# Kernel tuning notes

Hardware: AMD Instinct MI355X
Metric: run time of the kernel (lower is better)

Reference implementation:

```python
import jax, jax.numpy as jnp
import numpy as np

B, U, V = 2, 32, 2048
IN_DIM, STATE, CODE = 256, 512, 256
H, HD = 8, 64
INNER = H * HD  # 512
HID = STATE     # ffn capacity_factor = 1.0


def layernorm(x, g, b, eps=1e-5):
    mu = jnp.mean(x, axis=-1, keepdims=True)
    var = jnp.var(x, axis=-1, keepdims=True)
    return (x - mu) * jax.lax.rsqrt(var + eps) * g + b


def setup_inputs() -> dict:
    key = jax.random.key(0)
    ks = jax.random.split(key, 24)
    s = 0.02
    inp = {
        'receiver_states': jax.random.normal(ks[0], (B, U, STATE), jnp.float32),
        'receiver_signatures': jax.random.normal(ks[1], (B, U, 64), jnp.float32),
        'receiver_codes': jax.random.normal(ks[2], (B, U, CODE), jnp.float32),
        'sender_states': jax.random.normal(ks[3], (B, V, IN_DIM), jnp.float32),
        # layernorms
        'ln_s_g': jnp.ones((IN_DIM,), jnp.float32), 'ln_s_b': jnp.zeros((IN_DIM,), jnp.float32),
        'ln_r_g': jnp.ones((STATE,), jnp.float32), 'ln_r_b': jnp.zeros((STATE,), jnp.float32),
        # ModFC query: in=STATE out=INNER ctx=CODE
        'Wq': jax.random.normal(ks[4], (INNER, STATE), jnp.float32) * s,
        'bq': jnp.zeros((INNER,), jnp.float32),
        'Cq': jax.random.normal(ks[5], (STATE, CODE), jnp.float32) * s,
        # ModFC key/value: in=IN_DIM out=INNER ctx=CODE
        'Wk': jax.random.normal(ks[6], (INNER, IN_DIM), jnp.float32) * s,
        'bk': jnp.zeros((INNER,), jnp.float32),
        'Ck': jax.random.normal(ks[7], (IN_DIM, CODE), jnp.float32) * s,
        'Wv': jax.random.normal(ks[8], (INNER, IN_DIM), jnp.float32) * s,
        'bv': jnp.zeros((INNER,), jnp.float32),
        'Cv': jax.random.normal(ks[9], (IN_DIM, CODE), jnp.float32) * s,
        # exit ModFC: in=INNER out=STATE ctx=CODE
        'We': jax.random.normal(ks[10], (STATE, INNER), jnp.float32) * s,
        'be': jnp.zeros((STATE,), jnp.float32),
        'Ce': jax.random.normal(ks[11], (INNER, CODE), jnp.float32) * s,
        'ls_attn': jnp.ones((STATE,), jnp.float32) * 1.0,
        # FFN
        'ln_f_g': jnp.ones((STATE,), jnp.float32), 'ln_f_b': jnp.zeros((STATE,), jnp.float32),
        'W1': jax.random.normal(ks[12], (HID, STATE), jnp.float32) * s,
        'b1': jnp.zeros((HID,), jnp.float32),
        'C1': jax.random.normal(ks[13], (STATE, CODE), jnp.float32) * s,
        'W2': jax.random.normal(ks[14], (STATE, HID), jnp.float32) * s,
        'b2': jnp.zeros((STATE,), jnp.float32),
        'C2': jax.random.normal(ks[15], (HID, CODE), jnp.float32) * s,
        'ls_ffn': jnp.ones((STATE,), jnp.float32) * 1e-6,
    }
    return inp


def reference(receiver_states, receiver_signatures, receiver_codes, sender_states,
              ln_s_g, ln_s_b, ln_r_g, ln_r_b,
              Wq, bq, Cq, Wk, bk, Ck, Wv, bv, Cv, We, be, Ce, ls_attn,
              ln_f_g, ln_f_b, W1, b1, C1, W2, b2, C2, ls_ffn):
    codes = receiver_codes  # (b,u,code)
    # --- ReadInAttention ---
    r_ln = layernorm(receiver_states, ln_r_g, ln_r_b)           # (b,u,state)
    s_ln = layernorm(sender_states, ln_s_g, ln_s_b)             # (b,v,in)
    # ModFC: y = linear(x * (1 + code @ C))
    # queries: (b,u,inner)
    q = jnp.einsum('bus,is->bui', r_ln * (1.0 + jnp.einsum('buc,sc->bus', codes, Cq)), Wq) + bq
    # per-receiver modulated senders: scale (b,u,in) broadcast over v
    scale_k = 1.0 + jnp.einsum('buc,ic->bui', codes, Ck)        # (b,u,in)
    scale_v = 1.0 + jnp.einsum('buc,ic->bui', codes, Cv)        # (b,u,in)
    mod_k = s_ln[:, :, None, :] * scale_k[:, None, :, :]        # (b,v,u,in)
    mod_v = s_ln[:, :, None, :] * scale_v[:, None, :, :]        # (b,v,u,in)
    keys = jnp.einsum('bvui,oi->bvuo', mod_k, Wk) + bk          # (b,v,u,inner)
    values = jnp.einsum('bvui,oi->bvuo', mod_v, Wv) + bv        # (b,v,u,inner)
    keys = keys.reshape(B, V, U, H, HD).transpose(0, 3, 2, 1, 4)    # (b,h,u,v,c)
    values = values.reshape(B, V, U, H, HD).transpose(0, 3, 2, 1, 4)
    qh = q.reshape(B, U, H, HD).transpose(0, 2, 1, 3)           # (b,h,u,c)
    scores = jnp.einsum('bhuc,bhuvc->bhuv', qh, keys) / np.sqrt(HD)
    attn = jax.nn.softmax(scores, axis=-1)
    msg = jnp.einsum('bhuv,bhuvc->bhuc', attn, values)          # (b,h,u,c)
    msg = msg.transpose(0, 2, 1, 3).reshape(B, U, INNER)        # (b,u,inner)
    msg = jnp.einsum('bui,oi->buo', msg * (1.0 + jnp.einsum('buc,ic->bui', codes, Ce)), We) + be
    attn_out = msg * ls_attn  # include_residual=False in read-in attention
    # --- ModFFN (residual) ---
    x = attn_out
    r = layernorm(x, ln_f_g, ln_f_b)
    h1 = jnp.einsum('bus,os->buo', r * (1.0 + jnp.einsum('buc,sc->bus', codes, C1)), W1) + b1
    h1 = jax.nn.gelu(h1, approximate=False)
    h2 = jnp.einsum('buh,oh->buo', h1 * (1.0 + jnp.einsum('buc,hc->buh', codes, C2)), W2) + b2
    out = x + h2 * ls_ffn
    return out
```

## Files before the change

### kernel.cpp

```cpp
#include <hip/hip_runtime.h>
#include <math.h>

#define B_ 2
#define U_ 32
#define V_ 2048
#define IN_ 256
#define ST_ 512
#define H_ 8
#define BU_ 64
#define NR_ 512

#define WS_SLN   0u
#define WS_SLNT  1048576u
#define WS_SCALE 2097152u
#define WS_T     2260992u
#define WS_CB    2392064u
#define WS_SSUMP 2392576u
#define WS_CTXP  2396672u
#define WS_AO    3445248u
#define WS_H2    3478016u
#define WS_AOP   3510784u

__device__ __forceinline__ float wsum(float v){
  #pragma unroll
  for(int m=32;m>0;m>>=1) v += __shfl_xor(v, m, 64);
  return v;
}

#define FMA4(A, t, S) { A.x += (t)*(S).x; A.y += (t)*(S).y; A.z += (t)*(S).z; A.w += (t)*(S).w; }

__global__ __launch_bounds__(256) void k_pre(const float* __restrict__ snd,
    const float* __restrict__ g, const float* __restrict__ bb,
    const float* __restrict__ codes,
    const float* __restrict__ Cq, const float* __restrict__ Ck, const float* __restrict__ Cv,
    const float* __restrict__ Ce, const float* __restrict__ C1, const float* __restrict__ C2,
    float* __restrict__ ws){
  __shared__ float tile[32][261];
  __shared__ float cds[8][256];
  const int tid = threadIdx.x;
  if(blockIdx.x < 128){
    const int wave = tid>>6, lane = tid&63;
    const int rowbase = blockIdx.x * 32;
    const int b = rowbase >> 11, vloc = rowbase & 2047;
    float4 gg  = *(const float4*)(g  + lane*4);
    float4 bbv = *(const float4*)(bb + lane*4);
    for(int it=0; it<8; ++it){
      int rl = it*4 + wave;
      int r  = rowbase + rl;
      float4 x = *(const float4*)(snd + (size_t)r*IN_ + lane*4);
      float s = x.x+x.y+x.z+x.w;
      float q = x.x*x.x+x.y*x.y+x.z*x.z+x.w*x.w;
      s = wsum(s); q = wsum(q);
      float mu = s*(1.0f/256.0f);
      float rv = rsqrtf(q*(1.0f/256.0f) - mu*mu + 1e-5f);
      float4 y;
      y.x = (x.x-mu)*rv*gg.x + bbv.x;
      y.y = (x.y-mu)*rv*gg.y + bbv.y;
      y.z = (x.z-mu)*rv*gg.z + bbv.z;
      y.w = (x.w-mu)*rv*gg.w + bbv.w;
      *(float4*)(ws + WS_SLN + (size_t)r*IN_ + lane*4) = y;
      tile[rl][lane*4+0] = y.x;
      tile[rl][lane*4+1] = y.y;
      tile[rl][lane*4+2] = y.z;
      tile[rl][lane*4+3] = y.w;
    }
    __syncthreads();
    const int vh = tid & 31;
    const int ibase = (tid >> 5);
    for(int it=0; it<32; ++it){
      int i = it*8 + ibase;
      ws[WS_SLNT + ((size_t)b*IN_ + i)*V_ + vloc + vh] = tile[vh][i];
    }
  } else {
    const int idx = blockIdx.x - 128;
    const int cg = idx % 40, bg = idx / 40;
    #pragma unroll
    for(int j=0;j<8;++j){
      int fi = j*256 + tid;
      cds[fi>>8][fi&255] = codes[(size_t)(bg*8)*256 + fi];
    }
    __syncthreads();
    const int q = tid & 3;
    const int col = cg*64 + (tid >> 2);
    const float* Cp; int loc;
    if(col < 512){ Cp = Cq; loc = col; }
    else if(col < 768){ Cp = Ck; loc = col - 512; }
    else if(col < 1024){ Cp = Cv; loc = col - 768; }
    else if(col < 1536){ Cp = Ce; loc = col - 1024; }
    else if(col < 2048){ Cp = C1; loc = col - 1536; }
    else { Cp = C2; loc = col - 2048; }
    const float4* wrow = (const float4*)(Cp + (size_t)loc*256 + q*64);
    float acc[8] = {0,0,0,0,0,0,0,0};
    #pragma unroll 4
    for(int i=0;i<16;++i){
      float4 w = wrow[i];
      #pragma unroll
      for(int k=0;k<8;++k){
        const float4 c = *(const float4*)(&cds[k][q*64 + i*4]);
        acc[k] += w.x*c.x + w.y*c.y + w.z*c.z + w.w*c.w;
      }
    }
    #pragma unroll
    for(int k=0;k<8;++k){
      acc[k] += __shfl_xor(acc[k], 1, 64);
      acc[k] += __shfl_xor(acc[k], 2, 64);
    }
    ws[WS_SCALE + (size_t)(bg*8 + q)*2560 + col]     = 1.0f + acc[q];
    ws[WS_SCALE + (size_t)(bg*8 + q + 4)*2560 + col] = 1.0f + acc[q+4];
  }
}

__global__ __launch_bounds__(256) void k_qt(const float* __restrict__ rst,
    const float* __restrict__ lg, const float* __restrict__ lb,
    const float* __restrict__ Wq, const float* __restrict__ bq,
    const float* __restrict__ Wk, const float* __restrict__ bk,
    float* __restrict__ ws){
  const int bu = blockIdx.x >> 3, h = blockIdx.x & 7;
  const int b = bu >> 5, u = bu & 31;
  const int r = (b*8 + h)*32 + u;
  const int tid = threadIdx.x, wave = tid>>6, lane = tid&63;
  __shared__ float xm[512];
  __shared__ float qv[64];
  __shared__ float red[4][65];
  __shared__ float rsm[4], rqm[4];
  float2 x2 = *(const float2*)(rst + (size_t)bu*512 + tid*2);
  float s = x2.x + x2.y, q = x2.x*x2.x + x2.y*x2.y;
  s = wsum(s); q = wsum(q);
  if(lane==0){ rsm[wave] = s; rqm[wave] = q; }
  __syncthreads();
  float S = rsm[0]+rsm[1]+rsm[2]+rsm[3];
  float Q = rqm[0]+rqm[1]+rqm[2]+rqm[3];
  float mu = S*(1.0f/512.0f);
  float rv = rsqrtf(Q*(1.0f/512.0f) - mu*mu + 1e-5f);
  const float* scal = ws + WS_SCALE + (size_t)bu*2560;
  xm[tid*2]   = ((x2.x-mu)*rv*lg[tid*2]   + lb[tid*2])   * scal[tid*2];
  xm[tid*2+1] = ((x2.y-mu)*rv*lg[tid*2+1] + lb[tid*2+1]) * scal[tid*2+1];
  __syncthreads();
  {
    const int o = tid & 63, sp = tid >> 6;
    const float4* wq = (const float4*)(Wq + (size_t)(h*64 + o)*512 + sp*128);
    const float* xp = xm + sp*128;
    float acc = 0.f;
    #pragma unroll 8
    for(int c4=0;c4<32;++c4){
      float4 w = wq[c4];
      acc += w.x*xp[c4*4] + w.y*xp[c4*4+1] + w.z*xp[c4*4+2] + w.w*xp[c4*4+3];
    }
    red[sp][o] = acc;
  }
  __syncthreads();
  if(tid < 64)
    qv[tid] = red[0][tid]+red[1][tid]+red[2][tid]+red[3][tid] + bq[h*64+tid];
  __syncthreads();
  if(tid < 64){
    float p = qv[tid] * bk[h*64+tid];
    p = wsum(p);
    if(tid==0) ws[WS_CB + r] = p;
  }
  {
    float acc = 0.f;
    #pragma unroll 4
    for(int d=0; d<64; ++d)
      acc += qv[d] * Wk[(size_t)(h*64+d)*256 + tid];
    ws[WS_T + (size_t)r*256 + tid] = acc * scal[512 + tid];
  }
}

__global__ __launch_bounds__(512) void k_scctx(const float* __restrict__ Tm, float* __restrict__ ws){
  const int rg = blockIdx.x >> 3, vc = blockIdx.x & 7;
  const int r0 = rg * 16;
  const int b  = rg >> 4;
  const int v0 = vc * 256;
  const int tid = threadIdx.x, lane = tid & 63;
  const int w  = __builtin_amdgcn_readfirstlane(tid >> 6);
  const int wr = w & 1, wk = w >> 1;
  const int rw8 = wr * 8;
  const int i0 = lane * 4;
  const int srow = tid >> 6;
  const int sf   = (tid & 63) * 4;

  __shared__ float P[16][256];
  __shared__ float stg[32][256];

  float4 a0={0,0,0,0},a1={0,0,0,0},a2={0,0,0,0},a3={0,0,0,0};
  float4 a4={0,0,0,0},a5={0,0,0,0},a6={0,0,0,0},a7={0,0,0,0};

  const float* Trow = Tm + (size_t)(r0 + rw8)*256;

  const float* p1base = ws + WS_SLNT + (size_t)b*IN_*V_ + v0;
  float4 g0,g1,g2,g3;
  g0 = *(const float4*)(p1base + (size_t)(srow    )*V_ + sf);
  g1 = *(const float4*)(p1base + (size_t)(srow+ 8)*V_ + sf);
  g2 = *(const float4*)(p1base + (size_t)(srow+16)*V_ + sf);
  g3 = *(const float4*)(p1base + (size_t)(srow+24)*V_ + sf);
  for(int s=0; s<8; ++s){
    __syncthreads();
    *(float4*)&stg[srow   ][sf] = g0;
    *(float4*)&stg[srow+ 8][sf] = g1;
    *(float4*)&stg[srow+16][sf] = g2;
    *(float4*)&stg[srow+24][sf] = g3;
    if(s < 7){
      const float* nb = p1base + (size_t)(s+1)*32*V_;
      g0 = *(const float4*)(nb + (size_t)(srow    )*V_ + sf);
      g1 = *(const float4*)(nb + (size_t)(srow+ 8)*V_ + sf);
      g2 = *(const float4*)(nb + (size_t)(srow+16)*V_ + sf);
      g3 = *(const float4*)(nb + (size_t)(srow+24)*V_ + sf);
    }
    const int kgA = s*32 + wk*8;
    float4 tA[8], tB[8];
    #pragma unroll
    for(int j=0;j<8;++j) tA[j] = *(const float4*)(Trow + (size_t)j*256 + kgA);
    __syncthreads();
    #pragma unroll
    for(int j=0;j<8;++j) tB[j] = *(const float4*)(Trow + (size_t)j*256 + kgA + 4);
    {
      const int kl = wk*8;
      float4 s0 = *(const float4*)&stg[kl+0][i0];
      float4 s1 = *(const float4*)&stg[kl+1][i0];
      float4 s2 = *(const float4*)&stg[kl+2][i0];
      float4 s3 = *(const float4*)&stg[kl+3][i0];
      FMA4(a0,tA[0].x,s0) FMA4(a0,tA[0].y,s1) FMA4(a0,tA[0].z,s2) FMA4(a0,tA[0].w,s3)
      FMA4(a1,tA[1].x,s0) FMA4(a1,tA[1].y,s1) FMA4(a1,tA[1].z,s2) FMA4(a1,tA[1].w,s3)
      FMA4(a2,tA[2].x,s0) FMA4(a2,tA[2].y,s1) FMA4(a2,tA[2].z,s2) FMA4(a2,tA[2].w,s3)
      FMA4(a3,tA[3].x,s0) FMA4(a3,tA[3].y,s1) FMA4(a3,tA[3].z,s2) FMA4(a3,tA[3].w,s3)
      FMA4(a4,tA[4].x,s0) FMA4(a4,tA[4].y,s1) FMA4(a4,tA[4].z,s2) FMA4(a4,tA[4].w,s3)
      FMA4(a5,tA[5].x,s0) FMA4(a5,tA[5].y,s1) FMA4(a5,tA[5].z,s2) FMA4(a5,tA[5].w,s3)
      FMA4(a6,tA[6].x,s0) FMA4(a6,tA[6].y,s1) FMA4(a6,tA[6].z,s2) FMA4(a6,tA[6].w,s3)
      FMA4(a7,tA[7].x,s0) FMA4(a7,tA[7].y,s1) FMA4(a7,tA[7].z,s2) FMA4(a7,tA[7].w,s3)
    }
    {
      const int kl = wk*8 + 4;
      float4 s0 = *(const float4*)&stg[kl+0][i0];
      float4 s1 = *(const float4*)&stg[kl+1][i0];
      float4 s2 = *(const float4*)&stg[kl+2][i0];
      float4 s3 = *(const float4*)&stg[kl+3][i0];
      FMA4(a0,tB[0].x,s0) FMA4(a0,tB[0].y,s1) FMA4(a0,tB[0].z,s2) FMA4(a0,tB[0].w,s3)
      FMA4(a1,tB[1].x,s0) FMA4(a1,tB[1].y,s1) FMA4(a1,tB[1].z,s2) FMA4(a1,tB[1].w,s3)
      FMA4(a2,tB[2].x,s0) FMA4(a2,tB[2].y,s1) FMA4(a2,tB[2].z,s2) FMA4(a2,tB[2].w,s3)
      FMA4(a3,tB[3].x,s0) FMA4(a3,tB[3].y,s1) FMA4(a3,tB[3].z,s2) FMA4(a3,tB[3].w,s3)
      FMA4(a4,tB[4].x,s0) FMA4(a4,tB[4].y,s1) FMA4(a4,tB[4].z,s2) FMA4(a4,tB[4].w,s3)
      FMA4(a5,tB[5].x,s0) FMA4(a5,tB[5].y,s1) FMA4(a5,tB[5].z,s2) FMA4(a5,tB[5].w,s3)
      FMA4(a6,tB[6].x,s0) FMA4(a6,tB[6].y,s1) FMA4(a6,tB[6].z,s2) FMA4(a6,tB[6].w,s3)
      FMA4(a7,tB[7].x,s0) FMA4(a7,tB[7].y,s1) FMA4(a7,tB[7].z,s2) FMA4(a7,tB[7].w,s3)
    }
  }
  __syncthreads();
  if(wk == 0){
    *(float4*)&P[rw8+0][i0]=a0; *(float4*)&P[rw8+1][i0]=a1;
    *(float4*)&P[rw8+2][i0]=a2; *(float4*)&P[rw8+3][i0]=a3;
    *(float4*)&P[rw8+4][i0]=a4; *(float4*)&P[rw8+5][i0]=a5;
    *(float4*)&P[rw8+6][i0]=a6; *(float4*)&P[rw8+7][i0]=a7;
  } else if(wk == 1){
    *(float4*)&stg[rw8+0][i0]=a0; *(float4*)&stg[rw8+1][i0]=a1;
    *(float4*)&stg[rw8+2][i0]=a2; *(float4*)&stg[rw8+3][i0]=a3;
    *(float4*)&stg[rw8+4][i0]=a4; *(float4*)&stg[rw8+5][i0]=a5;
    *(float4*)&stg[rw8+6][i0]=a6; *(float4*)&stg[rw8+7][i0]=a7;
  } else if(wk == 2){
    *(float4*)&stg[16+rw8+0][i0]=a0; *(float4*)&stg[16+rw8+1][i0]=a1;
    *(float4*)&stg[16+rw8+2][i0]=a2; *(float4*)&stg[16+rw8+3][i0]=a3;
    *(float4*)&stg[16+rw8+4][i0]=a4; *(float4*)&stg[16+rw8+5][i0]=a5;
    *(float4*)&stg[16+rw8+6][i0]=a6; *(float4*)&stg[16+rw8+7][i0]=a7;
  }
  __syncthreads();
  if(wk == 3){
    float4 av[8] = {a0,a1,a2,a3,a4,a5,a6,a7};
    #pragma unroll
    for(int j=0;j<8;++j){
      const int r = r0 + rw8 + j;
      const float cb = ws[WS_CB + r];
      float4 q0 = *(const float4*)&P[rw8+j][i0];
      float4 q1 = *(const float4*)&stg[rw8+j][i0];
      float4 q2 = *(const float4*)&stg[16+rw8+j][i0];
      float4 e;
      e.x = __expf((av[j].x+q0.x+q1.x+q2.x+cb)*0.125f);
      e.y = __expf((av[j].y+q0.y+q1.y+q2.y+cb)*0.125f);
      e.z = __expf((av[j].z+q0.z+q1.z+q2.z+cb)*0.125f);
      e.w = __expf((av[j].w+q0.w+q1.w+q2.w+cb)*0.125f);
      *(float4*)&P[rw8+j][i0] = e;
      float ss = wsum(e.x+e.y+e.z+e.w);
      if(lane==0) ws[WS_SSUMP + (size_t)r*8 + vc] = ss;
    }
  }

  a0=make_float4(0,0,0,0); a1=a0; a2=a0; a3=a0; a4=a0; a5=a0; a6=a0; a7=a0;
  const float* p2base = ws + WS_SLN + ((size_t)b*V_ + v0)*IN_;
  g0 = *(const float4*)(p2base + (size_t)(srow    )*IN_ + sf);
  g1 = *(const float4*)(p2base + (size_t)(srow+ 8)*IN_ + sf);
  g2 = *(const float4*)(p2base + (size_t)(srow+16)*IN_ + sf);
  g3 = *(const float4*)(p2base + (size_t)(srow+24)*IN_ + sf);
  for(int sv=0; sv<8; ++sv){
    __syncthreads();
    *(float4*)&stg[srow   ][sf] = g0;
    *(float4*)&stg[srow+ 8][sf] = g1;
    *(float4*)&stg[srow+16][sf] = g2;
    *(float4*)&stg[srow+24][sf] = g3;
    if(sv < 7){
      const float* nb = p2base + (size_t)(sv+1)*32*IN_;
      g0 = *(const float4*)(nb + (size_t)(srow    )*IN_ + sf);
      g1 = *(const float4*)(nb + (size_t)(srow+ 8)*IN_ + sf);
      g2 = *(const float4*)(nb + (size_t)(srow+16)*IN_ + sf);
      g3 = *(const float4*)(nb + (size_t)(srow+24)*IN_ + sf);
    }
    __syncthreads();
    {
      const int vl = wk*8, vg = sv*32 + vl;
      float4 p0_ = *(const float4*)&P[rw8+0][vg];
      float4 p1_ = *(const float4*)&P[rw8+1][vg];
      float4 p2_ = *(const float4*)&P[rw8+2][vg];
      float4 p3_ = *(const float4*)&P[rw8+3][vg];
      float4 p4_ = *(const float4*)&P[rw8+4][vg];
      float4 p5_ = *(const float4*)&P[rw8+5][vg];
      float4 p6_ = *(const float4*)&P[rw8+6][vg];
      float4 p7_ = *(const float4*)&P[rw8+7][vg];
      float4 s0 = *(const float4*)&stg[vl+0][i0];
      float4 s1 = *(const float4*)&stg[vl+1][i0];
      float4 s2 = *(const float4*)&stg[vl+2][i0];
      float4 s3 = *(const float4*)&stg[vl+3][i0];
      FMA4(a0,p0_.x,s0) FMA4(a0,p0_.y,s1) FMA4(a0,p0_.z,s2) FMA4(a0,p0_.w,s3)
      FMA4(a1,p1_.x,s0) FMA4(a1,p1_.y,s1) FMA4(a1,p1_.z,s2) FMA4(a1,p1_.w,s3)
      FMA4(a2,p2_.x,s0) FMA4(a2,p2_.y,s1) FMA4(a2,p2_.z,s2) FMA4(a2,p2_.w,s3)
      FMA4(a3,p3_.x,s0) FMA4(a3,p3_.y,s1) FMA4(a3,p3_.z,s2) FMA4(a3,p3_.w,s3)
      FMA4(a4,p4_.x,s0) FMA4(a4,p4_.y,s1) FMA4(a4,p4_.z,s2) FMA4(a4,p4_.w,s3)
      FMA4(a5,p5_.x,s0) FMA4(a5,p5_.y,s1) FMA4(a5,p5_.z,s2) FMA4(a5,p5_.w,s3)
      FMA4(a6,p6_.x,s0) FMA4(a6,p6_.y,s1) FMA4(a6,p6_.z,s2) FMA4(a6,p6_.w,s3)
      FMA4(a7,p7_.x,s0) FMA4(a7,p7_.y,s1) FMA4(a7,p7_.z,s2) FMA4(a7,p7_.w,s3)
    }
    {
      const int vl = wk*8 + 4, vg = sv*32 + vl;
      float4 p0_ = *(const float4*)&P[rw8+0][vg];
      float4 p1_ = *(const float4*)&P[rw8+1][vg];
      float4 p2_ = *(const float4*)&P[rw8+2][vg];
      float4 p3_ = *(const float4*)&P[rw8+3][vg];
      float4 p4_ = *(const float4*)&P[rw8+4][vg];
      float4 p5_ = *(const float4*)&P[rw8+5][vg];
      float4 p6_ = *(const float4*)&P[rw8+6][vg];
      float4 p7_ = *(const float4*)&P[rw8+7][vg];
      float4 s0 = *(const float4*)&stg[vl+0][i0];
      float4 s1 = *(const float4*)&stg[vl+1][i0];
      float4 s2 = *(const float4*)&stg[vl+2][i0];
      float4 s3 = *(const float4*)&stg[vl+3][i0];
      FMA4(a0,p0_.x,s0) FMA4(a0,p0_.y,s1) FMA4(a0,p0_.z,s2) FMA4(a0,p0_.w,s3)
      FMA4(a1,p1_.x,s0) FMA4(a1,p1_.y,s1) FMA4(a1,p1_.z,s2) FMA4(a1,p1_.w,s3)
      FMA4(a2,p2_.x,s0) FMA4(a2,p2_.y,s1) FMA4(a2,p2_.z,s2) FMA4(a2,p2_.w,s3)
      FMA4(a3,p3_.x,s0) FMA4(a3,p3_.y,s1) FMA4(a3,p3_.z,s2) FMA4(a3,p3_.w,s3)
      FMA4(a4,p4_.x,s0) FMA4(a4,p4_.y,s1) FMA4(a4,p4_.z,s2) FMA4(a4,p4_.w,s3)
      FMA4(a5,p5_.x,s0) FMA4(a5,p5_.y,s1) FMA4(a5,p5_.z,s2) FMA4(a5,p5_.w,s3)
      FMA4(a6,p6_.x,s0) FMA4(a6,p6_.y,s1) FMA4(a6,p6_.z,s2) FMA4(a6,p6_.w,s3)
      FMA4(a7,p7_.x,s0) FMA4(a7,p7_.y,s1) FMA4(a7,p7_.z,s2) FMA4(a7,p7_.w,s3)
    }
  }
  __syncthreads();
  if(wk == 0){
    *(float4*)&P[rw8+0][i0]=a0; *(float4*)&P[rw8+1][i0]=a1;
    *(float4*)&P[rw8+2][i0]=a2; *(float4*)&P[rw8+3][i0]=a3;
    *(float4*)&P[rw8+4][i0]=a4; *(float4*)&P[rw8+5][i0]=a5;
    *(float4*)&P[rw8+6][i0]=a6; *(float4*)&P[rw8+7][i0]=a7;
  } else if(wk == 1){
    *(float4*)&stg[rw8+0][i0]=a0; *(float4*)&stg[rw8+1][i0]=a1;
    *(float4*)&stg[rw8+2][i0]=a2; *(float4*)&stg[rw8+3][i0]=a3;
    *(float4*)&stg[rw8+4][i0]=a4; *(float4*)&stg[rw8+5][i0]=a5;
    *(float4*)&stg[rw8+6][i0]=a6; *(float4*)&stg[rw8+7][i0]=a7;
  } else if(wk == 2){
    *(float4*)&stg[16+rw8+0][i0]=a0; *(float4*)&stg[16+rw8+1][i0]=a1;
    *(float4*)&stg[16+rw8+2][i0]=a2; *(float4*)&stg[16+rw8+3][i0]=a3;
    *(float4*)&stg[16+rw8+4][i0]=a4; *(float4*)&stg[16+rw8+5][i0]=a5;
    *(float4*)&stg[16+rw8+6][i0]=a6; *(float4*)&stg[16+rw8+7][i0]=a7;
  }
  __syncthreads();
  if(wk == 3){
    float4 av[8] = {a0,a1,a2,a3,a4,a5,a6,a7};
    #pragma unroll
    for(int j=0;j<8;++j){
      const int r = r0 + rw8 + j;
      float4 q0 = *(const float4*)&P[rw8+j][i0];
      float4 q1 = *(const float4*)&stg[rw8+j][i0];
      float4 q2 = *(const float4*)&stg[16+rw8+j][i0];
      float4 d;
      d.x = av[j].x+q0.x+q1.x+q2.x;
      d.y = av[j].y+q0.y+q1.y+q2.y;
      d.z = av[j].z+q0.z+q1.z+q2.z;
      d.w = av[j].w+q0.w+q1.w+q2.w;
      *(float4*)(ws + WS_CTXP + ((size_t)vc*NR_ + r)*IN_ + i0) = d;
    }
  }
}

__global__ __launch_bounds__(512) void k_mexit(const float* __restrict__ Wv, const float* __restrict__ bv,
    const float* __restrict__ We, float* __restrict__ ws){
  const int bu = blockIdx.x >> 2, st = blockIdx.x & 3;
  const int b = bu >> 5, u = bu & 31;
  const int tid = threadIdx.x;
  __shared__ float xs[2][256];
  __shared__ float m2s[128];
  __shared__ float ps[4][128];
  __shared__ float invS[2];
  if(tid < 2){
    const int r = (b*8 + st*2 + tid)*32 + u;
    float v = 0.f;
    #pragma unroll
    for(int k=0;k<8;++k) v += ws[WS_SSUMP + (size_t)r*8 + k];
    invS[tid] = 1.0f / v;
  }
  {
    const int hh = tid >> 8, i = tid & 255;
    const int r = (b*8 + st*2 + hh)*32 + u;
    float s = 0.f;
    #pragma unroll
    for(int vcx=0; vcx<8; ++vcx)
      s += ws[WS_CTXP + ((size_t)vcx*NR_ + r)*IN_ + i];
    xs[hh][i] = s * ws[WS_SCALE + (size_t)bu*2560 + 768 + i];
  }
  __syncthreads();
  {
    const int lo = tid & 127, sp = tid >> 7;
    const int o = st*128 + lo;
    const float4* wv = (const float4*)(Wv + (size_t)o*256 + sp*64);
    const float* xp = &xs[lo>>6][sp*64];
    float acc = 0.f;
    #pragma unroll
    for(int c4=0;c4<16;++c4){
      float4 w = wv[c4];
      acc += w.x*xp[c4*4]+w.y*xp[c4*4+1]+w.z*xp[c4*4+2]+w.w*xp[c4*4+3];
    }
    ps[sp][lo] = acc;
  }
  __syncthreads();
  if(tid < 128){
    const int o = st*128 + tid;
    m2s[tid] = ((ps[0][tid]+ps[1][tid]+ps[2][tid]+ps[3][tid]) * invS[tid>>6] + bv[o])
               * ws[WS_SCALE + (size_t)bu*2560 + 1024 + o];
  }
  __syncthreads();
  {
    const float4* we = (const float4*)(We + (size_t)tid*512 + st*128);
    float acc = 0.f;
    #pragma unroll 8
    for(int c4=0;c4<32;++c4){
      float4 w = we[c4];
      acc += w.x*m2s[c4*4]+w.y*m2s[c4*4+1]+w.z*m2s[c4*4+2]+w.w*m2s[c4*4+3];
    }
    ws[WS_AOP + ((size_t)st*BU_ + bu)*512 + tid] = acc;
  }
}

__global__ __launch_bounds__(256) void k_ffn1(const float* __restrict__ be, const float* __restrict__ lsa,
    const float* __restrict__ lg, const float* __restrict__ lb,
    const float* __restrict__ W1, const float* __restrict__ b1, float* __restrict__ ws){
  const int bu = blockIdx.x >> 2, ot = blockIdx.x & 3;
  const int tid = threadIdx.x, wave = tid>>6, lane = tid&63;
  __shared__ float xr[512];
  __shared__ float rsm[4], rqm[4];
  __shared__ float ps[2][128];
  const int s2 = tid*2;
  float2 x2;
  {
    const float* aop = ws + WS_AOP;
    float ax = aop[((size_t)0*BU_+bu)*512+s2] + aop[((size_t)1*BU_+bu)*512+s2]
             + aop[((size_t)2*BU_+bu)*512+s2] + aop[((size_t)3*BU_+bu)*512+s2];
    float ay = aop[((size_t)0*BU_+bu)*512+s2+1] + aop[((size_t)1*BU_+bu)*512+s2+1]
             + aop[((size_t)2*BU_+bu)*512+s2+1] + aop[((size_t)3*BU_+bu)*512+s2+1];
    x2.x = (ax + be[s2])   * lsa[s2];
    x2.y = (ay + be[s2+1]) * lsa[s2+1];
    *(float2*)(ws + WS_AO + (size_t)bu*512 + s2) = x2;
  }
  float s = x2.x+x2.y, q = x2.x*x2.x+x2.y*x2.y;
  s = wsum(s); q = wsum(q);
  if(lane==0){ rsm[wave]=s; rqm[wave]=q; }
  __syncthreads();
  float S=rsm[0]+rsm[1]+rsm[2]+rsm[3], Q=rqm[0]+rqm[1]+rqm[2]+rqm[3];
  float mu = S*(1.0f/512.0f);
  float rv = rsqrtf(Q*(1.0f/512.0f) - mu*mu + 1e-5f);
  const float* scal = ws + WS_SCALE + (size_t)bu*2560;
  xr[s2]   = ((x2.x-mu)*rv*lg[s2]   + lb[s2])   * scal[1536 + s2];
  xr[s2+1] = ((x2.y-mu)*rv*lg[s2+1] + lb[s2+1]) * scal[1536 + s2+1];
  __syncthreads();
  const int o = ot*128 + (tid & 127), sp = tid >> 7;
  const float4* w1 = (const float4*)(W1 + (size_t)o*512 + sp*256);
  const float* xp = xr + sp*256;
  float acc = 0.f;
  #pragma unroll 8
  for(int c4=0;c4<64;++c4){
    float4 w = w1[c4];
    acc += w.x*xp[c4*4]+w.y*xp[c4*4+1]+w.z*xp[c4*4+2]+w.w*xp[c4*4+3];
  }
  ps[sp][tid&127] = acc;
  __syncthreads();
  if(sp==0){
    float hh = ps[0][tid] + ps[1][tid] + b1[o];
    float ge = 0.5f*hh*(1.0f + erff(hh*0.70710678118654752f));
    ws[WS_H2 + (size_t)bu*512 + o] = ge * scal[2048 + o];
  }
}

__global__ __launch_bounds__(256) void k_ffn2(const float* __restrict__ W2, const float* __restrict__ b2,
    const float* __restrict__ lsf, const float* __restrict__ ws, float* __restrict__ out){
  const int bu = blockIdx.x >> 2, st = blockIdx.x & 3;
  const int tid = threadIdx.x;
  const int s = st*128 + (tid & 127), sp = tid >> 7;
  __shared__ float ps[2][128];
  const float4* w2 = (const float4*)(W2 + (size_t)s*512 + sp*256);
  const float* hp = ws + WS_H2 + (size_t)bu*512 + sp*256;
  float acc = 0.f;
  #pragma unroll 8
  for(int c4=0;c4<64;++c4){
    float4 w = w2[c4];
    acc += w.x*hp[c4*4]+w.y*hp[c4*4+1]+w.z*hp[c4*4+2]+w.w*hp[c4*4+3];
  }
  ps[sp][tid&127] = acc;
  __syncthreads();
  if(sp==0)
    out[(size_t)bu*512 + s] = ws[WS_AO + (size_t)bu*512 + s]
                            + (ps[0][tid]+ps[1][tid] + b2[s]) * lsf[s];
}

extern "C" void kernel_launch(void* const* d_in, const int* in_sizes, int n_in,
                              void* d_out, int out_size, void* d_ws, size_t ws_size,
                              hipStream_t stream) {
  (void)in_sizes; (void)n_in; (void)out_size; (void)ws_size;
  const float* rst   = (const float*)d_in[0];
  const float* codes = (const float*)d_in[2];
  const float* snd   = (const float*)d_in[3];
  const float* ln_s_g = (const float*)d_in[4];
  const float* ln_s_b = (const float*)d_in[5];
  const float* ln_r_g = (const float*)d_in[6];
  const float* ln_r_b = (const float*)d_in[7];
  const float* Wq = (const float*)d_in[8];
  const float* bq = (const float*)d_in[9];
  const float* Cq = (const float*)d_in[10];
  const float* Wk = (const float*)d_in[11];
  const float* bk = (const float*)d_in[12];
  const float* Ck = (const float*)d_in[13];
  const float* Wv = (const float*)d_in[14];
  const float* bv = (const float*)d_in[15];
  const float* Cv = (const float*)d_in[16];
  const float* We = (const float*)d_in[17];
  const float* be = (const float*)d_in[18];
  const float* Ce = (const float*)d_in[19];
  const float* lsa = (const float*)d_in[20];
  const float* ln_f_g = (const float*)d_in[21];
  const float* ln_f_b = (const float*)d_in[22];
  const float* W1 = (const float*)d_in[23];
  const float* b1 = (const float*)d_in[24];
  const float* C1 = (const float*)d_in[25];
  const float* W2 = (const float*)d_in[26];
  const float* b2 = (const float*)d_in[27];
  const float* C2 = (const float*)d_in[28];
  const float* lsf = (const float*)d_in[29];
  float* ws  = (float*)d_ws;
  float* out = (float*)d_out;

  k_pre   <<<448, 256, 0, stream>>>(snd, ln_s_g, ln_s_b, codes, Cq, Ck, Cv, Ce, C1, C2, ws);
  k_qt    <<<512, 256, 0, stream>>>(rst, ln_r_g, ln_r_b, Wq, bq, Wk, bk, ws);
  k_scctx <<<256, 512, 0, stream>>>((const float*)(ws + WS_T), ws);
  k_mexit <<<256, 512, 0, stream>>>(Wv, bv, We, ws);
  k_ffn1  <<<256, 256, 0, stream>>>(be, lsa, ln_f_g, ln_f_b, W1, b1, ws);
  k_ffn2  <<<256, 256, 0, stream>>>(W2, b2, lsf, ws, out);
}
```

Baseline: 97.60 us.

## Fuse query/T projection kernel into score-context kernel prologue

Result: slower. 149.0 us (+52.6%).

```diff
diff --git a/kernel.cpp b/kernel.cpp
--- a/kernel.cpp
+++ b/kernel.cpp
@@ -110,66 +110,17 @@
   }
 }
 
-__global__ __launch_bounds__(256) void k_qt(const float* __restrict__ rst,
+__global__ __launch_bounds__(512) void k_scctx(
+    const float* __restrict__ rst,
     const float* __restrict__ lg, const float* __restrict__ lb,
     const float* __restrict__ Wq, const float* __restrict__ bq,
     const float* __restrict__ Wk, const float* __restrict__ bk,
     float* __restrict__ ws){
-  const int bu = blockIdx.x >> 3, h = blockIdx.x & 7;
-  const int b = bu >> 5, u = bu & 31;
-  const int r = (b*8 + h)*32 + u;
-  const int tid = threadIdx.x, wave = tid>>6, lane = tid&63;
-  __shared__ float xm[512];
-  __shared__ float qv[64];
-  __shared__ float red[4][65];
-  __shared__ float rsm[4], rqm[4];
-  float2 x2 = *(const float2*)(rst + (size_t)bu*512 + tid*2);
-  float s = x2.x + x2.y, q = x2.x*x2.x + x2.y*x2.y;
-  s = wsum(s); q = wsum(q);
-  if(lane==0){ rsm[wave] = s; rqm[wave] = q; }
-  __syncthreads();
-  float S = rsm[0]+rsm[1]+rsm[2]+rsm[3];
-  float Q = rqm[0]+rqm[1]+rqm[2]+rqm[3];
-  float mu = S*(1.0f/512.0f);
-  float rv = rsqrtf(Q*(1.0f/512.0f) - mu*mu + 1e-5f);
-  const float* scal = ws + WS_SCALE + (size_t)bu*2560;
-  xm[tid*2]   = ((x2.x-mu)*rv*lg[tid*2]   + lb[tid*2])   * scal[tid*2];
-  xm[tid*2+1] = ((x2.y-mu)*rv*lg[tid*2+1] + lb[tid*2+1]) * scal[tid*2+1];
-  __syncthreads();
-  {
-    const int o = tid & 63, sp = tid >> 6;
-    const float4* wq = (const float4*)(Wq + (size_t)(h*64 + o)*512 + sp*128);
-    const float* xp = xm + sp*128;
-    float acc = 0.f;
-    #pragma unroll 8
-    for(int c4=0;c4<32;++c4){
-      float4 w = wq[c4];
-      acc += w.x*xp[c4*4] + w.y*xp[c4*4+1] + w.z*xp[c4*4+2] + w.w*xp[c4*4+3];
-    }
-    red[sp][o] = acc;
-  }
-  __syncthreads();
-  if(tid < 64)
-    qv[tid] = red[0][tid]+red[1][tid]+red[2][tid]+red[3][tid] + bq[h*64+tid];
-  __syncthreads();
-  if(tid < 64){
-    float p = qv[tid] * bk[h*64+tid];
-    p = wsum(p);
-    if(tid==0) ws[WS_CB + r] = p;
-  }
-  {
-    float acc = 0.f;
-    #pragma unroll 4
-    for(int d=0; d<64; ++d)
-      acc += qv[d] * Wk[(size_t)(h*64+d)*256 + tid];
-    ws[WS_T + (size_t)r*256 + tid] = acc * scal[512 + tid];
-  }
-}
-
-__global__ __launch_bounds__(512) void k_scctx(const float* __restrict__ Tm, float* __restrict__ ws){
   const int rg = blockIdx.x >> 3, vc = blockIdx.x & 7;
   const int r0 = rg * 16;
   const int b  = rg >> 4;
+  const int h  = (rg >> 1) & 7;
+  const int u0 = (rg & 1) * 16;
   const int v0 = vc * 256;
   const int tid = threadIdx.x, lane = tid & 63;
   const int w  = __builtin_amdgcn_readfirstlane(tid >> 6);
@@ -182,10 +133,95 @@
   __shared__ float P[16][256];
   __shared__ float stg[32][256];
 
+  {
+    float* xmF = &stg[0][0];
+    float* qvF = &P[0][0];
+    #pragma unroll
+    for(int rr=0; rr<2; ++rr){
+      const int j = w*2 + rr;
+      const int bu = b*32 + u0 + j;
+      const float* xr = rst + (size_t)bu*512 + lane*8;
+      float4 x0 = *(const float4*)(xr);
+      float4 x1 = *(const float4*)(xr + 4);
+      float s = x0.x+x0.y+x0.z+x0.w + x1.x+x1.y+x1.z+x1.w;
+      float q = x0.x*x0.x+x0.y*x0.y+x0.z*x0.z+x0.w*x0.w
+              + x1.x*x1.x+x1.y*x1.y+x1.z*x1.z+x1.w*x1.w;
+      s = wsum(s); q = wsum(q);
+      float mu = s*(1.0f/512.0f);
+      float rv = rsqrtf(q*(1.0f/512.0f) - mu*mu + 1e-5f);
+      const float* scq = ws + WS_SCALE + (size_t)bu*2560 + lane*8;
+      float4 sq0 = *(const float4*)(scq);
+      float4 sq1 = *(const float4*)(scq + 4);
+      float4 gg0 = *(const float4*)(lg + lane*8);
+      float4 gg1 = *(const float4*)(lg + lane*8 + 4);
+      float4 bb0 = *(const float4*)(lb + lane*8);
+      float4 bb1 = *(const float4*)(lb + lane*8 + 4);
+      float* dst = xmF + (size_t)j*512 + lane*8;
+      dst[0] = ((x0.x-mu)*rv*gg0.x + bb0.x) * sq0.x;
+      dst[1] = ((x0.y-mu)*rv*gg0.y + bb0.y) * sq0.y;
+      dst[2] = ((x0.z-mu)*rv*gg0.z + bb0.z) * sq0.z;
+      dst[3] = ((x0.w-mu)*rv*gg0.w + bb0.w) * sq0.w;
+      dst[4] = ((x1.x-mu)*rv*gg1.x + bb1.x) * sq1.x;
+      dst[5] = ((x1.y-mu)*rv*gg1.y + bb1.y) * sq1.y;
+      dst[6] = ((x1.z-mu)*rv*gg1.z + bb1.z) * sq1.z;
+      dst[7] = ((x1.w-mu)*rv*gg1.w + bb1.w) * sq1.w;
+    }
+    __syncthreads();
+    {
+      const int u = tid >> 5, o2 = tid & 31;
+      const float* xp = xmF + (size_t)u*512;
+      #pragma unroll
+      for(int oo=0; oo<2; ++oo){
+        const int o = o2*2 + oo;
+        const float4* wq = (const float4*)(Wq + (size_t)(h*64 + o)*512);
+        float acc = 0.f;
+        #pragma unroll 8
+        for(int c4=0; c4<128; ++c4){
+          float4 wv4 = wq[c4];
+          acc += wv4.x*xp[c4*4] + wv4.y*xp[c4*4+1] + wv4.z*xp[c4*4+2] + wv4.w*xp[c4*4+3];
+        }
+        qvF[u*65 + o] = acc + bq[h*64 + o];
+      }
+    }
+    __syncthreads();
+    if(tid < 64){
+      const int u = lane >> 2, dq = lane & 3;
+      float p = 0.f;
+      #pragma unroll
+      for(int dd=0; dd<16; ++dd){
+        const int d = dq*16 + dd;
+        p += qvF[u*65 + d] * bk[h*64 + d];
+      }
+      p += __shfl_xor(p, 1, 64);
+      p += __shfl_xor(p, 2, 64);
+      if(dq == 0) ws[WS_CB + r0 + u] = p;
+    }
+    {
+      const int u = tid >> 5, il = tid & 31;
+      const int bu = b*32 + u0 + u;
+      float4 acA = {0,0,0,0}, acB = {0,0,0,0};
+      #pragma unroll 4
+      for(int d=0; d<64; ++d){
+        const float qd = qvF[u*65 + d];
+        const float4* wk4 = (const float4*)(Wk + (size_t)(h*64 + d)*256 + il*8);
+        float4 w0 = wk4[0], w1 = wk4[1];
+        acA.x += qd*w0.x; acA.y += qd*w0.y; acA.z += qd*w0.z; acA.w += qd*w0.w;
+        acB.x += qd*w1.x; acB.y += qd*w1.y; acB.z += qd*w1.z; acB.w += qd*w1.w;
+      }
+      const float* sk = ws + WS_SCALE + (size_t)bu*2560 + 512 + il*8;
+      float4 s0 = *(const float4*)(sk), s1 = *(const float4*)(sk + 4);
+      acA.x*=s0.x; acA.y*=s0.y; acA.z*=s0.z; acA.w*=s0.w;
+      acB.x*=s1.x; acB.y*=s1.y; acB.z*=s1.z; acB.w*=s1.w;
+      float* tdst = ws + WS_T + (size_t)(r0 + u)*256 + il*8;
+      *(float4*)(tdst)     = acA;
+      *(float4*)(tdst + 4) = acB;
+    }
+    __syncthreads();
+  }
+
   float4 a0={0,0,0,0},a1={0,0,0,0},a2={0,0,0,0},a3={0,0,0,0};
   float4 a4={0,0,0,0},a5={0,0,0,0},a6={0,0,0,0},a7={0,0,0,0};
-
-  const float* Trow = Tm + (size_t)(r0 + rw8)*256;
+  const float* Trow = ws + WS_T + (size_t)(r0 + rw8)*256;
 
   const float* p1base = ws + WS_SLNT + (size_t)b*IN_*V_ + v0;
   float4 g0,g1,g2,g3;
@@ -302,31 +338,9 @@
       g3 = *(const float4*)(nb + (size_t)(srow+24)*IN_ + sf);
     }
     __syncthreads();
-    {
-      const int vl = wk*8, vg = sv*32 + vl;
-      float4 p0_ = *(const float4*)&P[rw8+0][vg];
-      float4 p1_ = *(const float4*)&P[rw8+1][vg];
-      float4 p2_ = *(const float4*)&P[rw8+2][vg];
-      float4 p3_ = *(const float4*)&P[rw8+3][vg];
-      float4 p4_ = *(const float4*)&P[rw8+4][vg];
-      float4 p5_ = *(const float4*)&P[rw8+5][vg];
-      float4 p6_ = *(const float4*)&P[rw8+6][vg];
-      float4 p7_ = *(const float4*)&P[rw8+7][vg];
-      float4 s0 = *(const float4*)&stg[vl+0][i0];
-      float4 s1 = *(const float4*)&stg[vl+1][i0];
-      float4 s2 = *(const float4*)&stg[vl+2][i0];
-      float4 s3 = *(const float4*)&stg[vl+3][i0];
-      FMA4(a0,p0_.x,s0) FMA4(a0,p0_.y,s1) FMA4(a0,p0_.z,s2) FMA4(a0,p0_.w,s3)
-      FMA4(a1,p1_.x,s0) FMA4(a1,p1_.y,s1) FMA4(a1,p1_.z,s2) FMA4(a1,p1_.w,s3)
-      FMA4(a2,p2_.x,s0) FMA4(a2,p2_.y,s1) FMA4(a2,p2_.z,s2) FMA4(a2,p2_.w,s3)
-      FMA4(a3,p3_.x,s0) FMA4(a3,p3_.y,s1) FMA4(a3,p3_.z,s2) FMA4(a3,p3_.w,s3)
-      FMA4(a4,p4_.x,s0) FMA4(a4,p4_.y,s1) FMA4(a4,p4_.z,s2) FMA4(a4,p4_.w,s3)
-      FMA4(a5,p5_.x,s0) FMA4(a5,p5_.y,s1) FMA4(a5,p5_.z,s2) FMA4(a5,p5_.w,s3)
-      FMA4(a6,p6_.x,s0) FMA4(a6,p6_.y,s1) FMA4(a6,p6_.z,s2) FMA4(a6,p6_.w,s3)
-      FMA4(a7,p7_.x,s0) FMA4(a7,p7_.y,s1) FMA4(a7,p7_.z,s2) FMA4(a7,p7_.w,s3)
-    }
-    {
-      const int vl = wk*8 + 4, vg = sv*32 + vl;
+    #pragma unroll
+    for(int half=0; half<2; ++half){
+      const int vl = wk*8 + half*4, vg = sv*32 + vl;
       float4 p0_ = *(const float4*)&P[rw8+0][vg];
       float4 p1_ = *(const float4*)&P[rw8+1][vg];
       float4 p2_ = *(const float4*)&P[rw8+2][vg];
@@ -550,8 +564,7 @@
   float* out = (float*)d_out;
 
   k_pre   <<<448, 256, 0, stream>>>(snd, ln_s_g, ln_s_b, codes, Cq, Ck, Cv, Ce, C1, C2, ws);
-  k_qt    <<<512, 256, 0, stream>>>(rst, ln_r_g, ln_r_b, Wq, bq, Wk, bk, ws);
-  k_scctx <<<256, 512, 0, stream>>>((const float*)(ws + WS_T), ws);
+  k_scctx <<<256, 512, 0, stream>>>(rst, ln_r_g, ln_r_b, Wq, bq, Wk, bk, ws);
   k_mexit <<<256, 512, 0, stream>>>(Wv, bv, We, ws);
   k_ffn1  <<<256, 256, 0, stream>>>(be, lsa, ln_f_g, ln_f_b, W1, b1, ws);
   k_ffn2  <<<256, 256, 0, stream>>>(W2, b2, lsf, ws, out);
```
